# Optimization experiments

Hardware: AMD Instinct MI355X
Metric: run time of the kernel (lower is better)

Reference implementation:

```python
import jax, jax.numpy as jnp
import numpy as np
from functools import partial

# Static configuration (must match setup_inputs / init_kwargs)
N_CLOUDS = 16      # number of point clouds in the batch
PTS = 16384        # points per cloud (uniform, batch vector is repeat(arange(B), PTS))
RATIO = 0.25       # EncodeLayer ratio
M = int(PTS * RATIO)  # samples per cloud = 4096


def _fps_one(p, m):
    """Farthest point sampling on one cloud p:[n,3] -> local indices [m].
    Matches torch_geometric fps with random_start=False semantics: start at point 0,
    then iteratively pick the point with max min-distance to the selected set."""
    d0 = jnp.sum((p - p[0]) ** 2, axis=-1)  # squared dist to first pick, [n]

    def step(dists, _):
        idx = jnp.argmax(dists)
        new_d = jnp.sum((p - p[idx]) ** 2, axis=-1)
        return jnp.minimum(dists, new_d), idx

    _, idxs = jax.lax.scan(step, d0, None, length=m - 1)
    return jnp.concatenate([jnp.zeros((1,), dtype=idxs.dtype), idxs])


def setup_inputs() -> dict:
    key = jax.random.key(0)
    k1, k2 = jax.random.split(key)
    pos = jax.random.normal(k1, (N_CLOUDS * PTS, 3), dtype=jnp.float32)
    feats = jax.random.normal(k2, (N_CLOUDS * PTS, 128), dtype=jnp.float32)
    batch = jnp.repeat(jnp.arange(N_CLOUDS, dtype=jnp.int64), PTS)
    return {"pos": pos, "feats": feats, "batch": batch}


def reference(pos, feats, batch):
    # pos:[N,3]; batch assumed uniform with N_CLOUDS clouds of PTS points each.
    pos_b = pos.reshape(N_CLOUDS, PTS, 3)
    local = jax.vmap(partial(_fps_one, m=M))(pos_b)  # [B, M] local indices
    offsets = (jnp.arange(N_CLOUDS, dtype=local.dtype) * PTS)[:, None]
    samples = (local + offsets).reshape(-1)  # global flat indices, like torch_geometric fps
    return samples
```

## Files before the change

kernel.cpp:

```cpp
#include <hip/hip_runtime.h>

#define N_CLOUDS 16
#define PTS      16384
#define M        4096
#define FPS_THREADS  1024
#define NWAVES   (FPS_THREADS / 64)
#define PPT      16
#define SORT_THREADS 512

typedef float v2f __attribute__((ext_vector_type(2)));
typedef unsigned long long u64;
typedef unsigned int u32;
typedef unsigned short u16;


#define PAIRS8_X(X) X(0) X(1) X(2) X(3) X(4) X(5) X(6) X(7)

#define DPP_MAX_STEP(key, CTRL) { \
        const u32 lo_  = (u32)(key); \
        const u32 hi_  = (u32)((key) >> 32); \
        const u32 lo2_ = (u32)__builtin_amdgcn_update_dpp(0, (int)lo_, (CTRL), 0xf, 0xf, false); \
        const u32 hi2_ = (u32)__builtin_amdgcn_update_dpp(0, (int)hi_, (CTRL), 0xf, 0xf, false); \
        const u64 ok_  = ((u64)hi2_ << 32) | lo2_; \
        (key) = (ok_ > (key)) ? ok_ : (key); \
    }

#define DPP_FMIN_STEP(v, CTRL) { \
        const int t_ = __builtin_amdgcn_update_dpp(__float_as_int(v), __float_as_int(v), (CTRL), 0xf, 0xf, false); \
        (v) = fminf((v), __int_as_float(t_)); \
    }
#define DPP_FMAX_STEP(v, CTRL) { \
        const int t_ = __builtin_amdgcn_update_dpp(__float_as_int(v), __float_as_int(v), (CTRL), 0xf, 0xf, false); \
        (v) = fmaxf((v), __int_as_float(t_)); \
    }
#define DPP_RED6(MACRO, v) \
        MACRO(v, 0x111) MACRO(v, 0x112) MACRO(v, 0x114) MACRO(v, 0x118) \
        MACRO(v, 0x142) MACRO(v, 0x143)

__global__ __launch_bounds__(SORT_THREADS)
void sort_kernel(const float* __restrict__ pos, float* __restrict__ pos_s,
                 u16* __restrict__ mapT)
{
    __shared__ u32 keys[PTS];
    const int cloud = blockIdx.x;
    const int tid   = threadIdx.x;
    const int ln    = tid & 63;
    const size_t b3 = (size_t)cloud * PTS * 3;

    float mnx = 1e30f, mxx = -1e30f, mny = 1e30f, mxy = -1e30f;
    for (int s = 0; s < PTS / SORT_THREADS; ++s) {
        const size_t o = b3 + (size_t)(tid + s * SORT_THREADS) * 3;
        const float x = pos[o + 0];
        const float y = pos[o + 1];
        mnx = fminf(mnx, x); mxx = fmaxf(mxx, x);
        mny = fminf(mny, y); mxy = fmaxf(mxy, y);
    }
    DPP_RED6(DPP_FMIN_STEP, mnx)
    DPP_RED6(DPP_FMAX_STEP, mxx)
    DPP_RED6(DPP_FMIN_STEP, mny)
    DPP_RED6(DPP_FMAX_STEP, mxy)
    float* red = (float*)keys;
    const int nw = SORT_THREADS / 64;
    if (ln == 63) {
        red[tid >> 6]          = mnx;
        red[nw + (tid >> 6)]   = mxx;
        red[2*nw + (tid >> 6)] = mny;
        red[3*nw + (tid >> 6)] = mxy;
    }
    __syncthreads();
    float xmin = red[0], xmax = red[nw], ymin = red[2*nw], ymax = red[3*nw];
    for (int w = 1; w < nw; ++w) {
        xmin = fminf(xmin, red[w]);
        xmax = fmaxf(xmax, red[nw + w]);
        ymin = fminf(ymin, red[2*nw + w]);
        ymax = fmaxf(ymax, red[3*nw + w]);
    }
    __syncthreads();

    const float xscale = 262143.0f / fmaxf(xmax - xmin, 1e-30f);
    const float yscale = 262143.0f / fmaxf(ymax - ymin, 1e-30f);
    for (int s = 0; s < PTS / SORT_THREADS; ++s) {
        const int i = tid + s * SORT_THREADS;
        const float x = pos[b3 + (size_t)i * 3];
        const u32 q = (u32)fminf(fmaxf((x - xmin) * xscale, 0.0f), 262143.0f);
        keys[i] = (q << 14) | (u32)i;
    }

    for (u32 k = 2; k <= (u32)PTS; k <<= 1) {
        for (u32 j = k >> 1; j; j >>= 1) {
            __syncthreads();
            for (int s = 0; s < PTS / SORT_THREADS; ++s) {
                const u32 i = (u32)(tid + s * SORT_THREADS);
                const u32 p = i ^ j;
                if (p > i) {
                    const u32 a = keys[i], b = keys[p];
                    if (((i & k) == 0) == (a > b)) { keys[i] = b; keys[p] = a; }
                }
            }
        }
    }
    __syncthreads();

    for (int s = 0; s < PTS / SORT_THREADS; ++s) {
        const int i = tid + s * SORT_THREADS;
        const u32 orig = keys[i] & (u32)(PTS - 1);
        const float y = pos[b3 + (size_t)orig * 3 + 1];
        const u32 q = (u32)fminf(fmaxf((y - ymin) * yscale, 0.0f), 262143.0f);
        keys[i] = (q << 14) | orig;
    }

    for (u32 k = 2; k <= 4096u; k <<= 1) {
        for (u32 j = k >> 1; j; j >>= 1) {
            __syncthreads();
            for (int s = 0; s < PTS / SORT_THREADS; ++s) {
                const u32 i = (u32)(tid + s * SORT_THREADS);
                const u32 p = i ^ j;
                if (p > i) {
                    const u32 a = keys[i], b = keys[p];
                    if (((i & k) == 0) == (a > b)) { keys[i] = b; keys[p] = a; }
                }
            }
        }
    }
    __syncthreads();

    for (int c = 0; c < 2; ++c) {
        u32 loc[PPT];
        const int cb = tid * 32 + c * PPT;
        for (int s = 0; s < PPT; ++s) loc[s] = keys[cb + s] & (u32)(PTS - 1);
        for (int a = 1; a < PPT; ++a) {
            const u32 v = loc[a];
            int b = a;
            while (b > 0 && loc[b - 1] > v) { loc[b] = loc[b - 1]; --b; }
            loc[b] = v;
        }
        for (int s = 0; s < PPT; ++s) keys[cb + s] = loc[s];
    }
    __syncthreads();

    for (int s = 0; s < PTS / SORT_THREADS; ++s) {
        const int i = tid + s * SORT_THREADS;
        const u32 orig = keys[i];
        mapT[(size_t)cloud * PTS + (size_t)(i & (PPT - 1)) * FPS_THREADS + (i >> 4)] = (u16)orig;
        const size_t so = b3 + (size_t)i * 3;
        const size_t oo = b3 + (size_t)orig * 3;
        pos_s[so + 0] = pos[oo + 0];
        pos_s[so + 1] = pos[oo + 1];
        pos_s[so + 2] = pos[oo + 2];
    }
}

template<bool SORTED>
__global__ __launch_bounds__(FPS_THREADS)
__attribute__((amdgpu_waves_per_eu(4, 4)))
void fps_kernel(const float* __restrict__ pos,
                const float* __restrict__ psrc,
                const u16* __restrict__ mapT,
                int* __restrict__ out)
{
#pragma clang fp contract(off)
    const int cloud = blockIdx.x;
    const int tid   = threadIdx.x;
    const int base  = cloud * PTS;
    const int wave  = tid >> 6;
    const int lane  = tid & 63;

    __shared__ u64 skey[2][NWAVES];
    __shared__ __attribute__((aligned(16))) u16 mlds[PTS];

    if constexpr (SORTED) {
        const uint4* src = (const uint4*)(mapT + (size_t)cloud * PTS);
        uint4* dst = (uint4*)mlds;
#pragma unroll
        for (int s = 0; s < PTS * 2 / 16 / FPS_THREADS; ++s)
            dst[s * FPS_THREADS + tid] = src[s * FPS_THREADS + tid];
        __syncthreads();
    }

    const float q0x = pos[(size_t)base * 3 + 0];
    const float q0y = pos[(size_t)base * 3 + 1];
    const float q0z = pos[(size_t)base * 3 + 2];
    v2f qx2 = {q0x, q0x}, qy2 = {q0y, q0y}, qz2 = {q0z, q0z};

    const float4* pos4 = (const float4*)psrc;
    const int fo = cloud * (PTS * 3 / 4) + tid * (PPT * 3 / 4);

#define DECL(j) v2f XX##j, YY##j, ZZ##j, DD##j;
    PAIRS8_X(DECL)
#undef DECL

#define QUADLOAD(q, j0, j1) { \
        const float4 fa = pos4[fo + 3*(q) + 0]; \
        const float4 fb = pos4[fo + 3*(q) + 1]; \
        const float4 fc = pos4[fo + 3*(q) + 2]; \
        XX##j0 = (v2f){fa.x, fa.w}; \
        YY##j0 = (v2f){fa.y, fb.x}; \
        ZZ##j0 = (v2f){fa.z, fb.y}; \
        XX##j1 = (v2f){fb.z, fc.y}; \
        YY##j1 = (v2f){fb.w, fc.z}; \
        ZZ##j1 = (v2f){fc.x, fc.w}; }
    QUADLOAD(0, 0, 1) QUADLOAD(1, 2, 3) QUADLOAD(2, 4, 5) QUADLOAD(3, 6, 7)
#undef QUADLOAD

#define PIN8(a,b,c,d,e,g,h,k) asm volatile("" : "+v"(a),"+v"(b),"+v"(c),"+v"(d),"+v"(e),"+v"(g),"+v"(h),"+v"(k));
    PIN8(XX0, XX1, XX2, XX3, XX4, XX5, XX6, XX7)
    PIN8(YY0, YY1, YY2, YY3, YY4, YY5, YY6, YY7)
    PIN8(ZZ0, ZZ1, ZZ2, ZZ3, ZZ4, ZZ5, ZZ6, ZZ7)
#undef PIN8

    float wxlo, wxhi, wylo, wyhi;
    {
        float mnx = fminf(XX0.x, XX0.y), mxx = fmaxf(XX0.x, XX0.y);
        float mny = fminf(YY0.x, YY0.y), mxy = fmaxf(YY0.x, YY0.y);
#define MINMAX(j) { mnx = fminf(mnx, fminf(XX##j.x, XX##j.y)); \
                    mxx = fmaxf(mxx, fmaxf(XX##j.x, XX##j.y)); \
                    mny = fminf(mny, fminf(YY##j.x, YY##j.y)); \
                    mxy = fmaxf(mxy, fmaxf(YY##j.x, YY##j.y)); }
        MINMAX(1) MINMAX(2) MINMAX(3) MINMAX(4) MINMAX(5) MINMAX(6) MINMAX(7)
#undef MINMAX
        DPP_RED6(DPP_FMIN_STEP, mnx)
        DPP_RED6(DPP_FMAX_STEP, mxx)
        DPP_RED6(DPP_FMIN_STEP, mny)
        DPP_RED6(DPP_FMAX_STEP, mxy)
        wxlo = __int_as_float(__builtin_amdgcn_readlane(__float_as_int(mnx), 63));
        wxhi = __int_as_float(__builtin_amdgcn_readlane(__float_as_int(mxx), 63));
        wylo = __int_as_float(__builtin_amdgcn_readlane(__float_as_int(mny), 63));
        wyhi = __int_as_float(__builtin_amdgcn_readlane(__float_as_int(mxy), 63));
    }

    float bd = -1.0f;
    int   bk = 0;
#define INITP(j) { \
        v2f dx = XX##j - qx2; \
        v2f dy = YY##j - qy2; \
        v2f dz = ZZ##j - qz2; \
        v2f nd = (dx * dx + dy * dy) + dz * dz; \
        DD##j = nd; \
        if (nd.x > bd) { bd = nd.x; bk = 2*(j); } \
        if (nd.y > bd) { bd = nd.y; bk = 2*(j) + 1; } \
    }
    PAIRS8_X(INITP)
#undef INITP

    if (tid == 0) out[cloud * M] = base;

    u32 c_hi, c_lo;
    {
        int bi;
        if constexpr (SORTED) bi = (int)mlds[(bk << 10) + tid];
        else                  bi = tid * PPT + bk;
        u64 key = ((u64)__float_as_uint(bd) << 32) | (u32)(~bi);
        DPP_MAX_STEP(key, 0x111)
        DPP_MAX_STEP(key, 0x112)
        DPP_MAX_STEP(key, 0x114)
        DPP_MAX_STEP(key, 0x118)
        DPP_MAX_STEP(key, 0x142)
        DPP_MAX_STEP(key, 0x143)
        c_hi = (u32)__builtin_amdgcn_readlane((int)(u32)(key >> 32), 63);
        c_lo = (u32)__builtin_amdgcn_readlane((int)(u32)key, 63);
    }

    for (int i = 1; i < M; ++i) {
        if (lane == 0) skey[i & 1][wave] = ((u64)c_hi << 32) | c_lo;
        __syncthreads();

        u64 key2 = skey[i & 1][lane & 15];
        DPP_MAX_STEP(key2, 0x111)
        DPP_MAX_STEP(key2, 0x112)
        DPP_MAX_STEP(key2, 0x114)
        DPP_MAX_STEP(key2, 0x118)
        const u32 wlo = (u32)__builtin_amdgcn_readlane((int)(u32)key2, 15);
        const int wi  = (int)(~wlo);

        if (tid == 0) out[cloud * M + i] = base + wi;

        const float* qp = pos + (size_t)(base + wi) * 3;
        const float qx = qp[0], qy = qp[1], qz = qp[2];

        const float dxg = fmaxf(fmaxf(wxlo - qx, qx - wxhi), 0.0f);
        const float dyg = fmaxf(fmaxf(wylo - qy, qy - wyhi), 0.0f);
        const float lb  = (dxg * dxg + dyg * dyg) * 0.9999f;
        if (!(lb > __uint_as_float(c_hi))) {
            qx2 = (v2f){qx, qx}; qy2 = (v2f){qy, qy}; qz2 = (v2f){qz, qz};
            bd = -1.0f; bk = 0;
#define UPD(j) { \
        v2f dx = XX##j - qx2; \
        v2f dy = YY##j - qy2; \
        v2f dz = ZZ##j - qz2; \
        v2f nd = (dx * dx + dy * dy) + dz * dz; \
        DD##j.x = fminf(DD##j.x, nd.x); \
        DD##j.y = fminf(DD##j.y, nd.y); \
        if (DD##j.x > bd) { bd = DD##j.x; bk = 2*(j); } \
        if (DD##j.y > bd) { bd = DD##j.y; bk = 2*(j) + 1; } \
    }
            PAIRS8_X(UPD)
#undef UPD
            int bi;
            if constexpr (SORTED) bi = (int)mlds[(bk << 10) + tid];
            else                  bi = tid * PPT + bk;
            u64 key = ((u64)__float_as_uint(bd) << 32) | (u32)(~bi);
            DPP_MAX_STEP(key, 0x111)
            DPP_MAX_STEP(key, 0x112)
            DPP_MAX_STEP(key, 0x114)
            DPP_MAX_STEP(key, 0x118)
            DPP_MAX_STEP(key, 0x142)
            DPP_MAX_STEP(key, 0x143)
            c_hi = (u32)__builtin_amdgcn_readlane((int)(u32)(key >> 32), 63);
            c_lo = (u32)__builtin_amdgcn_readlane((int)(u32)key, 63);
        }
    }
}

extern "C" void kernel_launch(void* const* d_in, const int* in_sizes, int n_in,
                              void* d_out, int out_size, void* d_ws, size_t ws_size,
                              hipStream_t stream) {
    const float* pos = (const float*)d_in[0];
    int* out = (int*)d_out;

    const size_t pos_s_bytes = (size_t)N_CLOUDS * PTS * 3 * sizeof(float);
    const size_t map_bytes   = (size_t)N_CLOUDS * PTS * sizeof(u16);
    if (d_ws && ws_size >= pos_s_bytes + map_bytes) {
        float* pos_s = (float*)d_ws;
        u16*   mapT  = (u16*)((char*)d_ws + pos_s_bytes);
        sort_kernel<<<N_CLOUDS, SORT_THREADS, 0, stream>>>(pos, pos_s, mapT);
        fps_kernel<true><<<N_CLOUDS, FPS_THREADS, 0, stream>>>(pos, pos_s, mapT, out);
    } else {
        fps_kernel<false><<<N_CLOUDS, FPS_THREADS, 0, stream>>>(pos, pos, nullptr, out);
    }
}
```

Before: 4.186 ms.

## Use 3D Morton ordering and 3D wave bounding boxes for FPS pruning

Replaces the two-pass x-then-y bitonic sort with a single sort keyed on an 18-bit 3D Morton code, so each wave owns a spatially compact 3D cell. The per-wave bounding box used for the skip test now includes z, which tightens the lower bound and lets more waves skip the distance update. This removes one bitonic sort pass and its extra keying pass. The cost is a few extra z min/max reductions and a coarser 64-level quantisation per axis.

```diff
diff --git a/kernel.cpp b/kernel.cpp
--- a/kernel.cpp
+++ b/kernel.cpp
@@ -36,6 +36,16 @@
 #define DPP_RED6(MACRO, v) \
         MACRO(v, 0x111) MACRO(v, 0x112) MACRO(v, 0x114) MACRO(v, 0x118) \
         MACRO(v, 0x142) MACRO(v, 0x143)
+
+__device__ __forceinline__ u32 spread3(u32 v) {
+    u32 r = (v & 1u);
+    r |= (v & 2u)  << 2;
+    r |= (v & 4u)  << 4;
+    r |= (v & 8u)  << 6;
+    r |= (v & 16u) << 8;
+    r |= (v & 32u) << 10;
+    return r;
+}
 
 __global__ __launch_bounds__(SORT_THREADS)
 void sort_kernel(const float* __restrict__ pos, float* __restrict__ pos_s,
@@ -48,17 +58,22 @@
     const size_t b3 = (size_t)cloud * PTS * 3;
 
     float mnx = 1e30f, mxx = -1e30f, mny = 1e30f, mxy = -1e30f;
+    float mnz = 1e30f, mxz = -1e30f;
     for (int s = 0; s < PTS / SORT_THREADS; ++s) {
         const size_t o = b3 + (size_t)(tid + s * SORT_THREADS) * 3;
         const float x = pos[o + 0];
         const float y = pos[o + 1];
+        const float z = pos[o + 2];
         mnx = fminf(mnx, x); mxx = fmaxf(mxx, x);
         mny = fminf(mny, y); mxy = fmaxf(mxy, y);
+        mnz = fminf(mnz, z); mxz = fmaxf(mxz, z);
     }
     DPP_RED6(DPP_FMIN_STEP, mnx)
     DPP_RED6(DPP_FMAX_STEP, mxx)
     DPP_RED6(DPP_FMIN_STEP, mny)
     DPP_RED6(DPP_FMAX_STEP, mxy)
+    DPP_RED6(DPP_FMIN_STEP, mnz)
+    DPP_RED6(DPP_FMAX_STEP, mxz)
     float* red = (float*)keys;
     const int nw = SORT_THREADS / 64;
     if (ln == 63) {
@@ -66,50 +81,36 @@
         red[nw + (tid >> 6)]   = mxx;
         red[2*nw + (tid >> 6)] = mny;
         red[3*nw + (tid >> 6)] = mxy;
+        red[4*nw + (tid >> 6)] = mnz;
+        red[5*nw + (tid >> 6)] = mxz;
     }
     __syncthreads();
     float xmin = red[0], xmax = red[nw], ymin = red[2*nw], ymax = red[3*nw];
+    float zmin = red[4*nw], zmax = red[5*nw];
     for (int w = 1; w < nw; ++w) {
         xmin = fminf(xmin, red[w]);
         xmax = fmaxf(xmax, red[nw + w]);
         ymin = fminf(ymin, red[2*nw + w]);
         ymax = fmaxf(ymax, red[3*nw + w]);
+        zmin = fminf(zmin, red[4*nw + w]);
+        zmax = fmaxf(zmax, red[5*nw + w]);
     }
     __syncthreads();
 
-    const float xscale = 262143.0f / fmaxf(xmax - xmin, 1e-30f);
-    const float yscale = 262143.0f / fmaxf(ymax - ymin, 1e-30f);
+    const float xscale = 63.999f / fmaxf(xmax - xmin, 1e-30f);
+    const float yscale = 63.999f / fmaxf(ymax - ymin, 1e-30f);
+    const float zscale = 63.999f / fmaxf(zmax - zmin, 1e-30f);
     for (int s = 0; s < PTS / SORT_THREADS; ++s) {
         const int i = tid + s * SORT_THREADS;
-        const float x = pos[b3 + (size_t)i * 3];
-        const u32 q = (u32)fminf(fmaxf((x - xmin) * xscale, 0.0f), 262143.0f);
-        keys[i] = (q << 14) | (u32)i;
+        const size_t o = b3 + (size_t)i * 3;
+        const u32 qx = (u32)fminf(fmaxf((pos[o + 0] - xmin) * xscale, 0.0f), 63.0f);
+        const u32 qy = (u32)fminf(fmaxf((pos[o + 1] - ymin) * yscale, 0.0f), 63.0f);
+        const u32 qz = (u32)fminf(fmaxf((pos[o + 2] - zmin) * zscale, 0.0f), 63.0f);
+        const u32 m = spread3(qx) | (spread3(qy) << 1) | (spread3(qz) << 2);
+        keys[i] = (m << 14) | (u32)i;
     }
 
     for (u32 k = 2; k <= (u32)PTS; k <<= 1) {
-        for (u32 j = k >> 1; j; j >>= 1) {
-            __syncthreads();
-            for (int s = 0; s < PTS / SORT_THREADS; ++s) {
-                const u32 i = (u32)(tid + s * SORT_THREADS);
-                const u32 p = i ^ j;
-                if (p > i) {
-                    const u32 a = keys[i], b = keys[p];
-                    if (((i & k) == 0) == (a > b)) { keys[i] = b; keys[p] = a; }
-                }
-            }
-        }
-    }
-    __syncthreads();
-
-    for (int s = 0; s < PTS / SORT_THREADS; ++s) {
-        const int i = tid + s * SORT_THREADS;
-        const u32 orig = keys[i] & (u32)(PTS - 1);
-        const float y = pos[b3 + (size_t)orig * 3 + 1];
-        const u32 q = (u32)fminf(fmaxf((y - ymin) * yscale, 0.0f), 262143.0f);
-        keys[i] = (q << 14) | orig;
-    }
-
-    for (u32 k = 2; k <= 4096u; k <<= 1) {
         for (u32 j = k >> 1; j; j >>= 1) {
             __syncthreads();
             for (int s = 0; s < PTS / SORT_THREADS; ++s) {
@@ -208,24 +209,31 @@
     PIN8(ZZ0, ZZ1, ZZ2, ZZ3, ZZ4, ZZ5, ZZ6, ZZ7)
 #undef PIN8
 
-    float wxlo, wxhi, wylo, wyhi;
+    float wxlo, wxhi, wylo, wyhi, wzlo, wzhi;
     {
         float mnx = fminf(XX0.x, XX0.y), mxx = fmaxf(XX0.x, XX0.y);
         float mny = fminf(YY0.x, YY0.y), mxy = fmaxf(YY0.x, YY0.y);
+        float mnz = fminf(ZZ0.x, ZZ0.y), mxz = fmaxf(ZZ0.x, ZZ0.y);
 #define MINMAX(j) { mnx = fminf(mnx, fminf(XX##j.x, XX##j.y)); \
                     mxx = fmaxf(mxx, fmaxf(XX##j.x, XX##j.y)); \
                     mny = fminf(mny, fminf(YY##j.x, YY##j.y)); \
-                    mxy = fmaxf(mxy, fmaxf(YY##j.x, YY##j.y)); }
+                    mxy = fmaxf(mxy, fmaxf(YY##j.x, YY##j.y)); \
+                    mnz = fminf(mnz, fminf(ZZ##j.x, ZZ##j.y)); \
+                    mxz = fmaxf(mxz, fmaxf(ZZ##j.x, ZZ##j.y)); }
         MINMAX(1) MINMAX(2) MINMAX(3) MINMAX(4) MINMAX(5) MINMAX(6) MINMAX(7)
 #undef MINMAX
         DPP_RED6(DPP_FMIN_STEP, mnx)
         DPP_RED6(DPP_FMAX_STEP, mxx)
         DPP_RED6(DPP_FMIN_STEP, mny)
         DPP_RED6(DPP_FMAX_STEP, mxy)
+        DPP_RED6(DPP_FMIN_STEP, mnz)
+        DPP_RED6(DPP_FMAX_STEP, mxz)
         wxlo = __int_as_float(__builtin_amdgcn_readlane(__float_as_int(mnx), 63));
         wxhi = __int_as_float(__builtin_amdgcn_readlane(__float_as_int(mxx), 63));
         wylo = __int_as_float(__builtin_amdgcn_readlane(__float_as_int(mny), 63));
         wyhi = __int_as_float(__builtin_amdgcn_readlane(__float_as_int(mxy), 63));
+        wzlo = __int_as_float(__builtin_amdgcn_readlane(__float_as_int(mnz), 63));
+        wzhi = __int_as_float(__builtin_amdgcn_readlane(__float_as_int(mxz), 63));
     }
 
     float bd = -1.0f;
@@ -279,7 +287,8 @@
 
         const float dxg = fmaxf(fmaxf(wxlo - qx, qx - wxhi), 0.0f);
         const float dyg = fmaxf(fmaxf(wylo - qy, qy - wyhi), 0.0f);
-        const float lb  = (dxg * dxg + dyg * dyg) * 0.9999f;
+        const float dzg = fmaxf(fmaxf(wzlo - qz, qz - wzhi), 0.0f);
+        const float lb  = (dxg * dxg + dyg * dyg + dzg * dzg) * 0.9999f;
         if (!(lb > __uint_as_float(c_hi))) {
             qx2 = (v2f){qx, qx}; qy2 = (v2f){qy, qy}; qz2 = (v2f){qz, qz};
             bd = -1.0f; bk = 0;
```

Result: slower. 5.524 ms (+32.0%).

## Add z-sort pass and per-row 3D bounding boxes for FPS pruning

Applied to the files above, without the earlier changes.

Adds a third bitonic pass sorting 1024-point chunks by z, so each 16-lane row owns a tighter spatial cell. FPS computes per-row x/y/z bounding boxes and per-row max distance, and skips the distance update when every row's lower bound exceeds its current max. The aim is to prune more distance updates per iteration. It costs an extra sort pass, and the all-rows condition may prune less often than the old per-wave check.

```diff
diff --git a/kernel.cpp b/kernel.cpp
--- a/kernel.cpp
+++ b/kernel.cpp
@@ -36,6 +36,24 @@
 #define DPP_RED6(MACRO, v) \
         MACRO(v, 0x111) MACRO(v, 0x112) MACRO(v, 0x114) MACRO(v, 0x118) \
         MACRO(v, 0x142) MACRO(v, 0x143)
+#define DPP_BFLY4(MACRO, v) \
+        MACRO(v, 0xB1) MACRO(v, 0x4E) MACRO(v, 0x141) MACRO(v, 0x140)
+
+#define BITONIC_PASS(KMAX) \
+    for (u32 k = 2; k <= (u32)(KMAX); k <<= 1) { \
+        for (u32 j = k >> 1; j; j >>= 1) { \
+            __syncthreads(); \
+            for (int s = 0; s < PTS / SORT_THREADS; ++s) { \
+                const u32 i = (u32)(tid + s * SORT_THREADS); \
+                const u32 p = i ^ j; \
+                if (p > i) { \
+                    const u32 a = keys[i], b = keys[p]; \
+                    if (((i & k) == 0) == (a > b)) { keys[i] = b; keys[p] = a; } \
+                } \
+            } \
+        } \
+    } \
+    __syncthreads();
 
 __global__ __launch_bounds__(SORT_THREADS)
 void sort_kernel(const float* __restrict__ pos, float* __restrict__ pos_s,
@@ -48,17 +66,22 @@
     const size_t b3 = (size_t)cloud * PTS * 3;
 
     float mnx = 1e30f, mxx = -1e30f, mny = 1e30f, mxy = -1e30f;
+    float mnz = 1e30f, mxz = -1e30f;
     for (int s = 0; s < PTS / SORT_THREADS; ++s) {
         const size_t o = b3 + (size_t)(tid + s * SORT_THREADS) * 3;
         const float x = pos[o + 0];
         const float y = pos[o + 1];
+        const float z = pos[o + 2];
         mnx = fminf(mnx, x); mxx = fmaxf(mxx, x);
         mny = fminf(mny, y); mxy = fmaxf(mxy, y);
+        mnz = fminf(mnz, z); mxz = fmaxf(mxz, z);
     }
     DPP_RED6(DPP_FMIN_STEP, mnx)
     DPP_RED6(DPP_FMAX_STEP, mxx)
     DPP_RED6(DPP_FMIN_STEP, mny)
     DPP_RED6(DPP_FMAX_STEP, mxy)
+    DPP_RED6(DPP_FMIN_STEP, mnz)
+    DPP_RED6(DPP_FMAX_STEP, mxz)
     float* red = (float*)keys;
     const int nw = SORT_THREADS / 64;
     if (ln == 63) {
@@ -66,40 +89,33 @@
         red[nw + (tid >> 6)]   = mxx;
         red[2*nw + (tid >> 6)] = mny;
         red[3*nw + (tid >> 6)] = mxy;
+        red[4*nw + (tid >> 6)] = mnz;
+        red[5*nw + (tid >> 6)] = mxz;
     }
     __syncthreads();
     float xmin = red[0], xmax = red[nw], ymin = red[2*nw], ymax = red[3*nw];
+    float zmin = red[4*nw], zmax = red[5*nw];
     for (int w = 1; w < nw; ++w) {
         xmin = fminf(xmin, red[w]);
         xmax = fmaxf(xmax, red[nw + w]);
         ymin = fminf(ymin, red[2*nw + w]);
         ymax = fmaxf(ymax, red[3*nw + w]);
+        zmin = fminf(zmin, red[4*nw + w]);
+        zmax = fmaxf(zmax, red[5*nw + w]);
     }
     __syncthreads();
 
     const float xscale = 262143.0f / fmaxf(xmax - xmin, 1e-30f);
     const float yscale = 262143.0f / fmaxf(ymax - ymin, 1e-30f);
+    const float zscale = 262143.0f / fmaxf(zmax - zmin, 1e-30f);
+
     for (int s = 0; s < PTS / SORT_THREADS; ++s) {
         const int i = tid + s * SORT_THREADS;
         const float x = pos[b3 + (size_t)i * 3];
         const u32 q = (u32)fminf(fmaxf((x - xmin) * xscale, 0.0f), 262143.0f);
         keys[i] = (q << 14) | (u32)i;
     }
-
-    for (u32 k = 2; k <= (u32)PTS; k <<= 1) {
-        for (u32 j = k >> 1; j; j >>= 1) {
-            __syncthreads();
-            for (int s = 0; s < PTS / SORT_THREADS; ++s) {
-                const u32 i = (u32)(tid + s * SORT_THREADS);
-                const u32 p = i ^ j;
-                if (p > i) {
-                    const u32 a = keys[i], b = keys[p];
-                    if (((i & k) == 0) == (a > b)) { keys[i] = b; keys[p] = a; }
-                }
-            }
-        }
-    }
-    __syncthreads();
+    BITONIC_PASS(PTS)
 
     for (int s = 0; s < PTS / SORT_THREADS; ++s) {
         const int i = tid + s * SORT_THREADS;
@@ -108,21 +124,16 @@
         const u32 q = (u32)fminf(fmaxf((y - ymin) * yscale, 0.0f), 262143.0f);
         keys[i] = (q << 14) | orig;
     }
-
-    for (u32 k = 2; k <= 4096u; k <<= 1) {
-        for (u32 j = k >> 1; j; j >>= 1) {
-            __syncthreads();
-            for (int s = 0; s < PTS / SORT_THREADS; ++s) {
-                const u32 i = (u32)(tid + s * SORT_THREADS);
-                const u32 p = i ^ j;
-                if (p > i) {
-                    const u32 a = keys[i], b = keys[p];
-                    if (((i & k) == 0) == (a > b)) { keys[i] = b; keys[p] = a; }
-                }
-            }
-        }
-    }
-    __syncthreads();
+    BITONIC_PASS(4096u)
+
+    for (int s = 0; s < PTS / SORT_THREADS; ++s) {
+        const int i = tid + s * SORT_THREADS;
+        const u32 orig = keys[i] & (u32)(PTS - 1);
+        const float z = pos[b3 + (size_t)orig * 3 + 2];
+        const u32 q = (u32)fminf(fmaxf((z - zmin) * zscale, 0.0f), 262143.0f);
+        keys[i] = (q << 14) | orig;
+    }
+    BITONIC_PASS(1024u)
 
     for (int c = 0; c < 2; ++c) {
         u32 loc[PPT];
@@ -149,6 +160,19 @@
         pos_s[so + 2] = pos[oo + 2];
     }
 }
+
+#define WAVE_REDUCE(key, rkhi, rklo, chi, clo) { \
+        DPP_MAX_STEP(key, 0xB1)   \
+        DPP_MAX_STEP(key, 0x4E)   \
+        DPP_MAX_STEP(key, 0x141)  \
+        DPP_MAX_STEP(key, 0x140)  \
+        rkhi = (u32)((key) >> 32); \
+        rklo = (u32)(key); \
+        DPP_MAX_STEP(key, 0x142)  \
+        DPP_MAX_STEP(key, 0x143)  \
+        chi = (u32)__builtin_amdgcn_readlane((int)(u32)((key) >> 32), 63); \
+        clo = (u32)__builtin_amdgcn_readlane((int)(u32)(key), 63); \
+    }
 
 template<bool SORTED>
 __global__ __launch_bounds__(FPS_THREADS)
@@ -208,24 +232,26 @@
     PIN8(ZZ0, ZZ1, ZZ2, ZZ3, ZZ4, ZZ5, ZZ6, ZZ7)
 #undef PIN8
 
-    float wxlo, wxhi, wylo, wyhi;
+    float rxlo, rxhi, rylo, ryhi, rzlo, rzhi;
     {
         float mnx = fminf(XX0.x, XX0.y), mxx = fmaxf(XX0.x, XX0.y);
         float mny = fminf(YY0.x, YY0.y), mxy = fmaxf(YY0.x, YY0.y);
+        float mnz = fminf(ZZ0.x, ZZ0.y), mxz = fmaxf(ZZ0.x, ZZ0.y);
 #define MINMAX(j) { mnx = fminf(mnx, fminf(XX##j.x, XX##j.y)); \
                     mxx = fmaxf(mxx, fmaxf(XX##j.x, XX##j.y)); \
                     mny = fminf(mny, fminf(YY##j.x, YY##j.y)); \
-                    mxy = fmaxf(mxy, fmaxf(YY##j.x, YY##j.y)); }
+                    mxy = fmaxf(mxy, fmaxf(YY##j.x, YY##j.y)); \
+                    mnz = fminf(mnz, fminf(ZZ##j.x, ZZ##j.y)); \
+                    mxz = fmaxf(mxz, fmaxf(ZZ##j.x, ZZ##j.y)); }
         MINMAX(1) MINMAX(2) MINMAX(3) MINMAX(4) MINMAX(5) MINMAX(6) MINMAX(7)
 #undef MINMAX
-        DPP_RED6(DPP_FMIN_STEP, mnx)
-        DPP_RED6(DPP_FMAX_STEP, mxx)
-        DPP_RED6(DPP_FMIN_STEP, mny)
-        DPP_RED6(DPP_FMAX_STEP, mxy)
-        wxlo = __int_as_float(__builtin_amdgcn_readlane(__float_as_int(mnx), 63));
-        wxhi = __int_as_float(__builtin_amdgcn_readlane(__float_as_int(mxx), 63));
-        wylo = __int_as_float(__builtin_amdgcn_readlane(__float_as_int(mny), 63));
-        wyhi = __int_as_float(__builtin_amdgcn_readlane(__float_as_int(mxy), 63));
+        DPP_BFLY4(DPP_FMIN_STEP, mnx)
+        DPP_BFLY4(DPP_FMAX_STEP, mxx)
+        DPP_BFLY4(DPP_FMIN_STEP, mny)
+        DPP_BFLY4(DPP_FMAX_STEP, mxy)
+        DPP_BFLY4(DPP_FMIN_STEP, mnz)
+        DPP_BFLY4(DPP_FMAX_STEP, mxz)
+        rxlo = mnx; rxhi = mxx; rylo = mny; ryhi = mxy; rzlo = mnz; rzhi = mxz;
     }
 
     float bd = -1.0f;
@@ -244,20 +270,13 @@
 
     if (tid == 0) out[cloud * M] = base;
 
-    u32 c_hi, c_lo;
+    u32 rk_hi, rk_lo, c_hi, c_lo;
     {
         int bi;
         if constexpr (SORTED) bi = (int)mlds[(bk << 10) + tid];
         else                  bi = tid * PPT + bk;
         u64 key = ((u64)__float_as_uint(bd) << 32) | (u32)(~bi);
-        DPP_MAX_STEP(key, 0x111)
-        DPP_MAX_STEP(key, 0x112)
-        DPP_MAX_STEP(key, 0x114)
-        DPP_MAX_STEP(key, 0x118)
-        DPP_MAX_STEP(key, 0x142)
-        DPP_MAX_STEP(key, 0x143)
-        c_hi = (u32)__builtin_amdgcn_readlane((int)(u32)(key >> 32), 63);
-        c_lo = (u32)__builtin_amdgcn_readlane((int)(u32)key, 63);
+        WAVE_REDUCE(key, rk_hi, rk_lo, c_hi, c_lo)
     }
 
     for (int i = 1; i < M; ++i) {
@@ -277,10 +296,11 @@
         const float* qp = pos + (size_t)(base + wi) * 3;
         const float qx = qp[0], qy = qp[1], qz = qp[2];
 
-        const float dxg = fmaxf(fmaxf(wxlo - qx, qx - wxhi), 0.0f);
-        const float dyg = fmaxf(fmaxf(wylo - qy, qy - wyhi), 0.0f);
-        const float lb  = (dxg * dxg + dyg * dyg) * 0.9999f;
-        if (!(lb > __uint_as_float(c_hi))) {
+        const float dxg = fmaxf(fmaxf(rxlo - qx, qx - rxhi), 0.0f);
+        const float dyg = fmaxf(fmaxf(rylo - qy, qy - ryhi), 0.0f);
+        const float dzg = fmaxf(fmaxf(rzlo - qz, qz - rzhi), 0.0f);
+        const float lb  = (dxg * dxg + dyg * dyg + dzg * dzg) * 0.9999f;
+        if (!__all(lb > __uint_as_float(rk_hi))) {
             qx2 = (v2f){qx, qx}; qy2 = (v2f){qy, qy}; qz2 = (v2f){qz, qz};
             bd = -1.0f; bk = 0;
 #define UPD(j) { \
@@ -299,14 +319,7 @@
             if constexpr (SORTED) bi = (int)mlds[(bk << 10) + tid];
             else                  bi = tid * PPT + bk;
             u64 key = ((u64)__float_as_uint(bd) << 32) | (u32)(~bi);
-            DPP_MAX_STEP(key, 0x111)
-            DPP_MAX_STEP(key, 0x112)
-            DPP_MAX_STEP(key, 0x114)
-            DPP_MAX_STEP(key, 0x118)
-            DPP_MAX_STEP(key, 0x142)
-            DPP_MAX_STEP(key, 0x143)
-            c_hi = (u32)__builtin_amdgcn_readlane((int)(u32)(key >> 32), 63);
-            c_lo = (u32)__builtin_amdgcn_readlane((int)(u32)key, 63);
+            WAVE_REDUCE(key, rk_hi, rk_lo, c_hi, c_lo)
         }
     }
 }
```

After: 4.400 ms. +5.1%, slower.
